# Kernel optimization log

Hardware: AMD Instinct MI355X
Metric: run time of the kernel (lower is better)

## Reference

```python
import jax, jax.numpy as jnp
import numpy as np

B, D, K = 131072, 64, 4096

def setup_inputs() -> dict:
    key = jax.random.key(0)
    k1, k2 = jax.random.split(key)
    z_e = jax.random.normal(k1, (B, D), dtype=jnp.float32)
    # nn.init.uniform_(-1/K, 1/K)
    codebook = jax.random.uniform(k2, (K, D), dtype=jnp.float32, minval=-1.0 / K, maxval=1.0 / K)
    return {"z_e": z_e, "codebook": codebook}

def reference(z_e, codebook):
    # squared-distance expansion: ||z||^2 + ||e||^2 - 2 z.e  -> (B, K)
    z2 = jnp.sum(z_e * z_e, axis=1, keepdims=True)          # (B, 1)
    e2 = jnp.sum(codebook * codebook, axis=1)[None, :]       # (1, K)
    ze = jnp.einsum('bd,kd->bk', z_e, codebook)              # (B, K)
    dist = z2 + e2 - 2.0 * ze
    codes = jnp.argmin(dist, axis=1)                         # (B,) int
    z_q = codebook[codes]                                    # (B, D) gather
    return (z_q, codes)
```

## Files before the change

### kernel.cpp

```cpp
#include <hip/hip_runtime.h>
#include <math.h>
#include <stdint.h>

#define Bn 131072
#define Dn 64
#define Kn 4096
#define TK 64
#define NKT (Kn / TK)
#define TPR 4
#define NRD (NKT / TPR)

typedef _Float16 f16x8 __attribute__((ext_vector_type(8)));
typedef float f32x4 __attribute__((ext_vector_type(4)));

__device__ __forceinline__ unsigned umn(unsigned a, unsigned b) { return a < b ? a : b; }
__device__ __forceinline__ unsigned umed3(unsigned a, unsigned b, unsigned c) {
  unsigned d;
  asm("v_med3_u32 %0, %1, %2, %3" : "=v"(d) : "v"(a), "v"(b), "v"(c));
  return d;
}

__device__ __forceinline__ void stage16(const void* g, void* l) {
  __builtin_amdgcn_global_load_lds((const __attribute__((address_space(1))) unsigned int*)g,
                                   (__attribute__((address_space(3))) unsigned int*)l,
                                   16, 0, 0);
}

__global__ __launch_bounds__(256) void cvt_cb(const float* __restrict__ cb,
                                              unsigned char* __restrict__ img) {
  int u = blockIdx.x * 256 + threadIdx.x;
  int g = u >> 3;
  int p = u & 7;
  int kt = g >> 6;
  int n = g & 63;
  const float4* s = (const float4*)(cb + (size_t)g * Dn + p * 8);
  float4 c0 = s[0], c1 = s[1];
  f16x8 h;
  h[0] = (_Float16)(c0.x * 4096.f); h[1] = (_Float16)(c0.y * 4096.f);
  h[2] = (_Float16)(c0.z * 4096.f); h[3] = (_Float16)(c0.w * 4096.f);
  h[4] = (_Float16)(c1.x * 4096.f); h[5] = (_Float16)(c1.y * 4096.f);
  h[6] = (_Float16)(c1.z * 4096.f); h[7] = (_Float16)(c1.w * 4096.f);
  *(f16x8*)(img + (size_t)kt * 8192 + n * 128 + ((p ^ (n & 7)) << 4)) = h;
}

template <int RB, int WB>
__device__ __forceinline__ void round_body(int rd, int tid,
                                           unsigned char* smem_,
                                           const unsigned char* b0,
                                           const unsigned char* b1,
                                           const unsigned char* wsrc,
                                           const f16x8 (&A)[2][2],
                                           unsigned (&k1)[2][4], unsigned (&k2)[2][4],
                                           unsigned (&tg)[4], const f32x4 c256) {
  asm volatile("s_waitcnt vmcnt(0)" ::: "memory");
  __builtin_amdgcn_s_barrier();
  __builtin_amdgcn_sched_barrier(0);
  if (rd + 1 < NRD) {
#pragma unroll
    for (int j = 0; j < TPR; ++j)
      stage16(wsrc + ((size_t)(rd + 1) * TPR + j) * 8192, smem_ + WB + j * 8192 + tid * 16);
  }
#pragma unroll
  for (int j = 0; j < TPR; ++j) {
#pragma unroll
    for (int t = 0; t < 4; ++t) {
      const f16x8 B0 = *(const f16x8*)(b0 + RB + j * 8192 + t * 2048);
      const f16x8 B1 = *(const f16x8*)(b1 + RB + j * 8192 + t * 2048);
      f32x4 a0 = __builtin_amdgcn_mfma_f32_16x16x32_f16(A[0][0], B0, c256, 0, 0, 0);
      f32x4 a1 = __builtin_amdgcn_mfma_f32_16x16x32_f16(A[1][0], B0, c256, 0, 0, 0);
      a0 = __builtin_amdgcn_mfma_f32_16x16x32_f16(A[0][1], B1, a0, 0, 0, 0);
      a1 = __builtin_amdgcn_mfma_f32_16x16x32_f16(A[1][1], B1, a1, 0, 0, 0);
#pragma unroll
      for (int r = 0; r < 4; ++r) {
        unsigned key0 = (__float_as_uint(a0[r]) & 0xFFFFFF00u) | tg[t];
        k2[0][r] = umed3(k1[0][r], k2[0][r], key0);
        k1[0][r] = umn(k1[0][r], key0);
        unsigned key1 = (__float_as_uint(a1[r]) & 0xFFFFFF00u) | tg[t];
        k2[1][r] = umed3(k1[1][r], k2[1][r], key1);
        k1[1][r] = umn(k1[1][r], key1);
      }
    }
#pragma unroll
    for (int t = 0; t < 4; ++t) tg[t] += 1;
  }
}

__global__ __launch_bounds__(512, 4) void vq_main(const float* __restrict__ z,
                                                  const float* __restrict__ cb,
                                                  const unsigned char* __restrict__ img,
                                                  float* __restrict__ out) {
  __shared__ __align__(16) unsigned char smem[66560];
  const int tid = threadIdx.x;
  const int lane = tid & 63;
  const int w = tid >> 6;
  const int q = lane >> 4;
  const int col = lane & 15;
  const int row0 = blockIdx.x * 256;

  const unsigned char* wsrc = img + tid * 16;
#pragma unroll
  for (int j = 0; j < TPR; ++j)
    stage16(wsrc + (size_t)j * 8192, smem + j * 8192 + tid * 16);

  f16x8 A[2][2];
#pragma unroll
  for (int i = 0; i < 2; ++i)
#pragma unroll
    for (int c = 0; c < 2; ++c) {
      const float* zp = z + (size_t)(row0 + w * 32 + i * 16 + col) * Dn + c * 32 + q * 8;
      float4 x0 = *(const float4*)zp;
      float4 x1 = *(const float4*)(zp + 4);
      f16x8 a;
      a[0] = (_Float16)(-2.f * x0.x); a[1] = (_Float16)(-2.f * x0.y);
      a[2] = (_Float16)(-2.f * x0.z); a[3] = (_Float16)(-2.f * x0.w);
      a[4] = (_Float16)(-2.f * x1.x); a[5] = (_Float16)(-2.f * x1.y);
      a[6] = (_Float16)(-2.f * x1.z); a[7] = (_Float16)(-2.f * x1.w);
      A[i][c] = a;
    }

  unsigned k1[2][4], k2[2][4];
#pragma unroll
  for (int i = 0; i < 2; ++i)
#pragma unroll
    for (int r = 0; r < 4; ++r) { k1[i][r] = 0xFFFFFFFFu; k2[i][r] = 0xFFFFFFFFu; }
  unsigned tg[4] = {0u << 6, 1u << 6, 2u << 6, 3u << 6};
  const f32x4 c256 = {256.f, 256.f, 256.f, 256.f};

  const int xu = (col & 7) << 4;
  const unsigned char* b0 = smem + col * 128 + ((q << 4) ^ xu);
  const unsigned char* b1 = smem + col * 128 + (((4 + q) << 4) ^ xu);

#pragma unroll 1
  for (int rp = 0; rp < NRD / 2; ++rp) {
    round_body<0, 32768>(2 * rp, tid, smem, b0, b1, wsrc, A, k1, k2, tg, c256);
    round_body<32768, 0>(2 * rp + 1, tid, smem, b0, b1, wsrc, A, k1, k2, tg, c256);
  }

  __syncthreads();
  unsigned* dmp = (unsigned*)smem;
#pragma unroll
  for (int i = 0; i < 2; ++i)
#pragma unroll
    for (int r = 0; r < 4; ++r) {
      int rb = w * 32 + i * 16 + q * 4 + r;
      dmp[rb * 33 + col * 2] = k1[i][r];
      dmp[rb * 33 + col * 2 + 1] = k2[i][r];
    }
  __syncthreads();

  {
    const int rl = tid >> 1;
    const int half = tid & 1;
    const unsigned* keys = dmp + rl * 33 + half * 16;
    unsigned mk = 0xFFFFFFFFu;
    for (int j = 0; j < 16; ++j) mk = umn(mk, keys[j]);
    const float lim = __uint_as_float(mk & 0xFFFFFF00u) + 0.5f;

    const float4* zr4 = (const float4*)(z + (size_t)(row0 + rl) * Dn);

    float r8[8];
#pragma unroll
    for (int g = 0; g < 2; ++g) {
      float4 v = zr4[g]; int j = g * 4;
      r8[j + 0] = __fmul_rn(v.x, v.x); r8[j + 1] = __fmul_rn(v.y, v.y);
      r8[j + 2] = __fmul_rn(v.z, v.z); r8[j + 3] = __fmul_rn(v.w, v.w);
    }
#pragma unroll
    for (int g = 2; g < 16; ++g) {
      float4 v = zr4[g]; int j = (g & 1) * 4;
      r8[j + 0] = __fadd_rn(r8[j + 0], __fmul_rn(v.x, v.x));
      r8[j + 1] = __fadd_rn(r8[j + 1], __fmul_rn(v.y, v.y));
      r8[j + 2] = __fadd_rn(r8[j + 2], __fmul_rn(v.z, v.z));
      r8[j + 3] = __fadd_rn(r8[j + 3], __fmul_rn(v.w, v.w));
    }
    float z2f = __fadd_rn(__fadd_rn(__fadd_rn(r8[0], r8[1]), __fadd_rn(r8[2], r8[3])),
                          __fadd_rn(__fadd_rn(r8[4], r8[5]), __fadd_rn(r8[6], r8[7])));

    float bq = INFINITY; int bc = Kn;
    for (int j = 0; j < 16; ++j) {
      unsigned key = keys[j];
      float sc = __uint_as_float(key & 0xFFFFFF00u);
      if (sc > lim) continue;
      int c2 = half * 16 + j;
      int tag = (int)(key & 0xFFu);
      int code = (tag & 63) * 64 + (tag >> 6) * 16 + (c2 >> 1);
      const float4* cr = (const float4*)(cb + (size_t)code * Dn);
      double ze = 0.0;
      float e8[8];
#pragma unroll
      for (int g = 0; g < 16; ++g) {
        float4 ev = cr[g]; float4 zv = zr4[g];
        ze += (double)ev.x * (double)zv.x + (double)ev.y * (double)zv.y +
              (double)ev.z * (double)zv.z + (double)ev.w * (double)zv.w;
        int jj = (g & 1) * 4;
        if (g < 2) {
          e8[jj + 0] = __fmul_rn(ev.x, ev.x); e8[jj + 1] = __fmul_rn(ev.y, ev.y);
          e8[jj + 2] = __fmul_rn(ev.z, ev.z); e8[jj + 3] = __fmul_rn(ev.w, ev.w);
        } else {
          e8[jj + 0] = __fadd_rn(e8[jj + 0], __fmul_rn(ev.x, ev.x));
          e8[jj + 1] = __fadd_rn(e8[jj + 1], __fmul_rn(ev.y, ev.y));
          e8[jj + 2] = __fadd_rn(e8[jj + 2], __fmul_rn(ev.z, ev.z));
          e8[jj + 3] = __fadd_rn(e8[jj + 3], __fmul_rn(ev.w, ev.w));
        }
      }
      float e2f = __fadd_rn(__fadd_rn(__fadd_rn(e8[0], e8[1]), __fadd_rn(e8[2], e8[3])),
                            __fadd_rn(__fadd_rn(e8[4], e8[5]), __fadd_rn(e8[6], e8[7])));
      float zef = (float)ze;
      float t1 = __fadd_rn(z2f, e2f);
      float t2 = __fmul_rn(2.0f, zef);
      float qv = __fadd_rn(t1, -t2);
      if (qv < bq || (qv == bq && code < bc)) { bq = qv; bc = code; }
    }
    float obq = __shfl_xor(bq, 1);
    int obc = __shfl_xor(bc, 1);
    if (obq < bq || (obq == bq && obc < bc)) { bq = obq; bc = obc; }
    if (half == 0) {
      ((int*)(smem + 65536))[rl] = bc;
      out[(size_t)Bn * Dn + row0 + rl] = (float)bc;
    }
  }
  __syncthreads();

  {
    const float4* cb4 = (const float4*)cb;
    float4* out4 = (float4*)out;
    const int* wc = (const int*)(smem + 65536);
#pragma unroll
    for (int i = 0; i < 8; ++i) {
      int t = i * 512 + tid;
      int r = t >> 4, c2 = t & 15;
      int wn = wc[r];
      out4[(size_t)(row0 + r) * 16 + c2] = cb4[(size_t)wn * 16 + c2];
    }
  }
}

extern "C" void kernel_launch(void* const* d_in, const int* in_sizes, int n_in,
                              void* d_out, int out_size, void* d_ws, size_t ws_size,
                              hipStream_t stream) {
  const float* z = (const float*)d_in[0];
  const float* cb = (const float*)d_in[1];
  float* out = (float*)d_out;
  unsigned char* img = (unsigned char*)d_ws;
  cvt_cb<<<128, 256, 0, stream>>>(cb, img);
  vq_main<<<Bn / 256, 512, 0, stream>>>(z, cb, img, out);
}
```

Measured before the change: 210.8 us.

## Double per-wave row tile to reuse each LDS codebook fragment across 64 rows

Each wave now covers 64 rows (four 16-row MFMA tiles) instead of 32, and blocks shrink from 512 to 256 threads while still handling 256 rows. Each LDS B fragment read therefore feeds four MFMAs instead of two, halving LDS read traffic per unit of compute. Each thread now does the full 32-candidate refinement for one row, which removes the shuffle merge. The cost is roughly double the accumulator and key registers per thread, fewer waves per CU (launch bounds 256,2), and twice the staging loads per thread.

```diff
diff --git a/kernel.cpp b/kernel.cpp
--- a/kernel.cpp
+++ b/kernel.cpp
@@ -49,16 +49,19 @@
                                            const unsigned char* b0,
                                            const unsigned char* b1,
                                            const unsigned char* wsrc,
-                                           const f16x8 (&A)[2][2],
-                                           unsigned (&k1)[2][4], unsigned (&k2)[2][4],
+                                           const f16x8 (&A)[4][2],
+                                           unsigned (&k1)[4][4], unsigned (&k2)[4][4],
                                            unsigned (&tg)[4], const f32x4 c256) {
   asm volatile("s_waitcnt vmcnt(0)" ::: "memory");
   __builtin_amdgcn_s_barrier();
   __builtin_amdgcn_sched_barrier(0);
   if (rd + 1 < NRD) {
 #pragma unroll
-    for (int j = 0; j < TPR; ++j)
-      stage16(wsrc + ((size_t)(rd + 1) * TPR + j) * 8192, smem_ + WB + j * 8192 + tid * 16);
+    for (int j = 0; j < TPR; ++j) {
+      const unsigned char* gs = wsrc + ((size_t)(rd + 1) * TPR + j) * 8192;
+      stage16(gs, smem_ + WB + j * 8192 + tid * 16);
+      stage16(gs + 4096, smem_ + WB + j * 8192 + 4096 + tid * 16);
+    }
   }
 #pragma unroll
   for (int j = 0; j < TPR; ++j) {
@@ -68,8 +71,12 @@
       const f16x8 B1 = *(const f16x8*)(b1 + RB + j * 8192 + t * 2048);
       f32x4 a0 = __builtin_amdgcn_mfma_f32_16x16x32_f16(A[0][0], B0, c256, 0, 0, 0);
       f32x4 a1 = __builtin_amdgcn_mfma_f32_16x16x32_f16(A[1][0], B0, c256, 0, 0, 0);
+      f32x4 a2 = __builtin_amdgcn_mfma_f32_16x16x32_f16(A[2][0], B0, c256, 0, 0, 0);
+      f32x4 a3 = __builtin_amdgcn_mfma_f32_16x16x32_f16(A[3][0], B0, c256, 0, 0, 0);
       a0 = __builtin_amdgcn_mfma_f32_16x16x32_f16(A[0][1], B1, a0, 0, 0, 0);
       a1 = __builtin_amdgcn_mfma_f32_16x16x32_f16(A[1][1], B1, a1, 0, 0, 0);
+      a2 = __builtin_amdgcn_mfma_f32_16x16x32_f16(A[2][1], B1, a2, 0, 0, 0);
+      a3 = __builtin_amdgcn_mfma_f32_16x16x32_f16(A[3][1], B1, a3, 0, 0, 0);
 #pragma unroll
       for (int r = 0; r < 4; ++r) {
         unsigned key0 = (__float_as_uint(a0[r]) & 0xFFFFFF00u) | tg[t];
@@ -78,6 +85,12 @@
         unsigned key1 = (__float_as_uint(a1[r]) & 0xFFFFFF00u) | tg[t];
         k2[1][r] = umed3(k1[1][r], k2[1][r], key1);
         k1[1][r] = umn(k1[1][r], key1);
+        unsigned key2 = (__float_as_uint(a2[r]) & 0xFFFFFF00u) | tg[t];
+        k2[2][r] = umed3(k1[2][r], k2[2][r], key2);
+        k1[2][r] = umn(k1[2][r], key2);
+        unsigned key3 = (__float_as_uint(a3[r]) & 0xFFFFFF00u) | tg[t];
+        k2[3][r] = umed3(k1[3][r], k2[3][r], key3);
+        k1[3][r] = umn(k1[3][r], key3);
       }
     }
 #pragma unroll
@@ -85,7 +98,7 @@
   }
 }
 
-__global__ __launch_bounds__(512, 4) void vq_main(const float* __restrict__ z,
+__global__ __launch_bounds__(256, 2) void vq_main(const float* __restrict__ z,
                                                   const float* __restrict__ cb,
                                                   const unsigned char* __restrict__ img,
                                                   float* __restrict__ out) {
@@ -99,15 +112,17 @@
 
   const unsigned char* wsrc = img + tid * 16;
 #pragma unroll
-  for (int j = 0; j < TPR; ++j)
+  for (int j = 0; j < TPR; ++j) {
     stage16(wsrc + (size_t)j * 8192, smem + j * 8192 + tid * 16);
-
-  f16x8 A[2][2];
-#pragma unroll
-  for (int i = 0; i < 2; ++i)
+    stage16(wsrc + (size_t)j * 8192 + 4096, smem + j * 8192 + 4096 + tid * 16);
+  }
+
+  f16x8 A[4][2];
+#pragma unroll
+  for (int i = 0; i < 4; ++i)
 #pragma unroll
     for (int c = 0; c < 2; ++c) {
-      const float* zp = z + (size_t)(row0 + w * 32 + i * 16 + col) * Dn + c * 32 + q * 8;
+      const float* zp = z + (size_t)(row0 + w * 64 + i * 16 + col) * Dn + c * 32 + q * 8;
       float4 x0 = *(const float4*)zp;
       float4 x1 = *(const float4*)(zp + 4);
       f16x8 a;
@@ -118,9 +133,9 @@
       A[i][c] = a;
     }
 
-  unsigned k1[2][4], k2[2][4];
-#pragma unroll
-  for (int i = 0; i < 2; ++i)
+  unsigned k1[4][4], k2[4][4];
+#pragma unroll
+  for (int i = 0; i < 4; ++i)
 #pragma unroll
     for (int r = 0; r < 4; ++r) { k1[i][r] = 0xFFFFFFFFu; k2[i][r] = 0xFFFFFFFFu; }
   unsigned tg[4] = {0u << 6, 1u << 6, 2u << 6, 3u << 6};
@@ -139,21 +154,20 @@
   __syncthreads();
   unsigned* dmp = (unsigned*)smem;
 #pragma unroll
-  for (int i = 0; i < 2; ++i)
+  for (int i = 0; i < 4; ++i)
 #pragma unroll
     for (int r = 0; r < 4; ++r) {
-      int rb = w * 32 + i * 16 + q * 4 + r;
+      int rb = w * 64 + i * 16 + q * 4 + r;
       dmp[rb * 33 + col * 2] = k1[i][r];
       dmp[rb * 33 + col * 2 + 1] = k2[i][r];
     }
   __syncthreads();
 
   {
-    const int rl = tid >> 1;
-    const int half = tid & 1;
-    const unsigned* keys = dmp + rl * 33 + half * 16;
+    const int rl = tid;
+    const unsigned* keys = dmp + rl * 33;
     unsigned mk = 0xFFFFFFFFu;
-    for (int j = 0; j < 16; ++j) mk = umn(mk, keys[j]);
+    for (int j = 0; j < 32; ++j) mk = umn(mk, keys[j]);
     const float lim = __uint_as_float(mk & 0xFFFFFF00u) + 0.5f;
 
     const float4* zr4 = (const float4*)(z + (size_t)(row0 + rl) * Dn);
@@ -177,13 +191,12 @@
                           __fadd_rn(__fadd_rn(r8[4], r8[5]), __fadd_rn(r8[6], r8[7])));
 
     float bq = INFINITY; int bc = Kn;
-    for (int j = 0; j < 16; ++j) {
+    for (int j = 0; j < 32; ++j) {
       unsigned key = keys[j];
       float sc = __uint_as_float(key & 0xFFFFFF00u);
       if (sc > lim) continue;
-      int c2 = half * 16 + j;
       int tag = (int)(key & 0xFFu);
-      int code = (tag & 63) * 64 + (tag >> 6) * 16 + (c2 >> 1);
+      int code = (tag & 63) * 64 + (tag >> 6) * 16 + (j >> 1);
       const float4* cr = (const float4*)(cb + (size_t)code * Dn);
       double ze = 0.0;
       float e8[8];
@@ -211,13 +224,8 @@
       float qv = __fadd_rn(t1, -t2);
       if (qv < bq || (qv == bq && code < bc)) { bq = qv; bc = code; }
     }
-    float obq = __shfl_xor(bq, 1);
-    int obc = __shfl_xor(bc, 1);
-    if (obq < bq || (obq == bq && obc < bc)) { bq = obq; bc = obc; }
-    if (half == 0) {
-      ((int*)(smem + 65536))[rl] = bc;
-      out[(size_t)Bn * Dn + row0 + rl] = (float)bc;
-    }
+    ((int*)(smem + 65536))[rl] = bc;
+    out[(size_t)Bn * Dn + row0 + rl] = (float)bc;
   }
   __syncthreads();
 
@@ -226,8 +234,8 @@
     float4* out4 = (float4*)out;
     const int* wc = (const int*)(smem + 65536);
 #pragma unroll
-    for (int i = 0; i < 8; ++i) {
-      int t = i * 512 + tid;
+    for (int i = 0; i < 16; ++i) {
+      int t = i * 256 + tid;
       int r = t >> 4, c2 = t & 15;
       int wn = wc[r];
       out4[(size_t)(row0 + r) * 16 + c2] = cb4[(size_t)wn * 16 + c2];
@@ -243,5 +251,5 @@
   float* out = (float*)d_out;
   unsigned char* img = (unsigned char*)d_ws;
   cvt_cb<<<128, 256, 0, stream>>>(cb, img);
-  vq_main<<<Bn / 256, 512, 0, stream>>>(z, cb, img, out);
-}
+  vq_main<<<Bn / 256, 256, 0, stream>>>(z, cb, img, out);
+}
```

After: 197.9 us. 6.1% less time.
